# Kernel optimization log

Measured on AMD Instinct MI355X. Metric: run time of the kernel, lower is better.

## Reference

```python
import jax, jax.numpy as jnp
import numpy as np

B, C, N, T = 16, 64, 1024, 64  # batch, channels (c_in==c_out), nodes, timesteps


def setup_inputs() -> dict:
    key = jax.random.key(0)
    k = jax.random.split(key, 5)
    return {
        "x": jax.random.normal(k[0], (B, C, N, T), dtype=jnp.float32),
        "w1": jax.random.uniform(k[1], (C, C), dtype=jnp.float32),  # (c_out, c_in)
        "b1": jax.random.uniform(k[2], (C, 1), dtype=jnp.float32),  # (c_in, 1) == (c_out, 1) since c_in==c_out
        "w2": jax.random.uniform(k[3], (C, C), dtype=jnp.float32),  # (c_out, c_out)
        "b2": jax.random.uniform(k[4], (C, 1), dtype=jnp.float32),  # (c_out, 1)
    }


def reference(x, w1, b1, w2, b2):
    b, c_in, n, t = x.shape
    c_out = w1.shape[0]
    # Input transform is time-independent: batch it over all timesteps at once.
    # (c_out, c_in) x (B, c_in, N, T) -> (T, B, c_out, N), then bias-add.
    xw = jnp.einsum('vf,bfnt->tbvn', w1, x) + b1  # b1 (C,1) broadcasts over (T,B,C,N)

    def step(h, xt):
        # h: (B, c_out, N); xt: (B, c_out, N)
        new_h = jnp.tanh(xt + jnp.einsum('vu,bun->bvn', w2, h) + b2)
        return new_h, new_h

    h0 = jnp.zeros((b, c_out, n), dtype=x.dtype)
    _, out = jax.lax.scan(step, h0, xw)  # out: (T, B, c_out, N)
    return jnp.moveaxis(out, 0, 3)  # (B, c_out, N, T)
```

## Files before the change

### kernel.cpp

```cpp
#include <hip/hip_runtime.h>
#include <hip/hip_bf16.h>

namespace {
constexpr int kB = 16, kC = 64, kN = 1024, kT = 64;
constexpr size_t kWsNeed = (size_t)kB * kC * kN * kT * 4;
}

typedef short bf16x8 __attribute__((ext_vector_type(8)));
typedef float f32x4 __attribute__((ext_vector_type(4)));

__device__ __forceinline__ float tanh_fast(float x) {
    float e = __expf(2.0f * x);
    return 1.0f - 2.0f * __builtin_amdgcn_rcpf(e + 1.0f);
}

__device__ __forceinline__ unsigned short bf16_rnd(float f) {
    unsigned int u = __float_as_uint(f);
    u = (u + 0x7FFFu + ((u >> 16) & 1u)) >> 16;
    return (unsigned short)u;
}
__device__ __forceinline__ float bf16_to_f32(unsigned short s) {
    return __uint_as_float(((unsigned int)s) << 16);
}
__device__ __forceinline__ void split3(float v, unsigned short& h,
                                       unsigned short& m, unsigned short& l) {
    h = bf16_rnd(v);
    float r = v - bf16_to_f32(h);
    m = bf16_rnd(r);
    float r2 = r - bf16_to_f32(m);
    l = bf16_rnd(r2);
}


__global__ __launch_bounds__(256, 2) void xw_gemm(
    const float* __restrict__ x, const float* __restrict__ w1,
    const float* __restrict__ b1, const float* __restrict__ b2,
    float* __restrict__ ws)
{
    __shared__ __align__(16) float w1t[64][72];
    __shared__ __align__(16) float xs[16][32][20];

    const int tid = threadIdx.x;
    const int bid = blockIdx.x;
    const int tc = bid & 3;
    const int nt = (bid >> 2) & 31;
    const int b  = bid >> 7;
    const int n0 = nt * 32;

    #pragma unroll
    for (int k = 0; k < 16; ++k) {
        int idx = tid + 256 * k;
        int v = idx >> 6, f = idx & 63;
        w1t[f][v] = w1[idx];
    }

    const int vg = tid >> 5;
    const int n  = tid & 31;
    const int v0 = vg * 8;
    const int p  = (n >> 3) & 3;

    float bias[8];
    #pragma unroll
    for (int vj = 0; vj < 8; ++vj) bias[vj] = b1[v0 + vj] + b2[v0 + vj];

    float acc[8][4][4];
    #pragma unroll
    for (int vj = 0; vj < 8; ++vj)
        #pragma unroll
        for (int q = 0; q < 4; ++q)
            #pragma unroll
            for (int j = 0; j < 4; ++j) acc[vj][q][j] = bias[vj];

    for (int fc = 0; fc < 4; ++fc) {
        __syncthreads();
        #pragma unroll
        for (int r = 0; r < 8; ++r) {
            int slot = tid + 256 * r;
            int f = slot >> 7, nn = (slot >> 2) & 31, tq = slot & 3;
            const float4 xv = *reinterpret_cast<const float4*>(
                x + ((size_t)(b * 64 + fc * 16 + f) * 1024 + n0 + nn) * 64
                  + tc * 16 + tq * 4);
            int pp = (nn >> 3) & 3;
            *reinterpret_cast<float4*>(&xs[f][nn][((tq ^ pp) * 4)]) = xv;
        }
        __syncthreads();

        for (int f = 0; f < 16; ++f) {
            const int ff = fc * 16 + f;
            const float4 wA = *reinterpret_cast<const float4*>(&w1t[ff][v0]);
            const float4 wB = *reinterpret_cast<const float4*>(&w1t[ff][v0 + 4]);
            float wv[8] = {wA.x, wA.y, wA.z, wA.w, wB.x, wB.y, wB.z, wB.w};
            #pragma unroll
            for (int q = 0; q < 4; ++q) {
                const float4 xv = *reinterpret_cast<const float4*>(&xs[f][n][q * 4]);
                float xe[4] = {xv.x, xv.y, xv.z, xv.w};
                #pragma unroll
                for (int vj = 0; vj < 8; ++vj)
                    #pragma unroll
                    for (int j = 0; j < 4; ++j)
                        acc[vj][q][j] = fmaf(wv[vj], xe[j], acc[vj][q][j]);
            }
        }
    }

    const int vt  = vg >> 1;
    const int m   = n >> 4;
    const int nl  = n & 15;
    const size_t tilecol = ((size_t)(b * 32 + nt) * 64) * 2048;
    #pragma unroll
    for (int q = 0; q < 4; ++q) {
        #pragma unroll
        for (int jj = 0; jj < 4; ++jj) {
            const int t = tc * 16 + ((q ^ p) * 4) + jj;
            #pragma unroll
            for (int half = 0; half < 2; ++half) {
                const int lane = nl + 16 * ((vg & 1) * 2 + half);
                float4 o;
                o.x = acc[half * 4 + 0][q][jj];
                o.y = acc[half * 4 + 1][q][jj];
                o.z = acc[half * 4 + 2][q][jj];
                o.w = acc[half * 4 + 3][q][jj];
                size_t off = tilecol + ((size_t)t * 8 + vt * 2 + m) * 256 + lane * 4;
                *reinterpret_cast<float4*>(ws + off) = o;
            }
        }
    }
}

__global__ __launch_bounds__(256, 2) void rnn_rec(
    const float* __restrict__ w2, const float* __restrict__ ws,
    float* __restrict__ out)
{
    __shared__ __align__(16) unsigned short hsp[3][32][72];

    const int tid  = threadIdx.x;
    const int w    = tid >> 6;
    const int lane = tid & 63;
    const int lg   = lane >> 4;
    const int nl   = lane & 15;
    const int bid  = blockIdx.x;
    const int nt   = bid & 31;
    const int b    = bid >> 5;
    const int n0   = nt * 32;

    for (int i = tid; i < 3456; i += 256)
        reinterpret_cast<unsigned int*>(hsp)[i] = 0u;

    bf16x8 aw[2][3];
    #pragma unroll
    for (int kc = 0; kc < 2; ++kc) {
        const float* src = w2 + (size_t)(16 * w + nl) * 64 + kc * 32 + lg * 8;
        float wv[8];
        #pragma unroll
        for (int j = 0; j < 8; ++j) wv[j] = src[j];
        #pragma unroll
        for (int j = 0; j < 8; ++j) {
            unsigned short h, m, l;
            split3(wv[j], h, m, l);
            aw[kc][0][j] = (short)h; aw[kc][1][j] = (short)m; aw[kc][2][j] = (short)l;
        }
    }

    const size_t slab = ((size_t)(b * 32 + nt) * 64) * 2048;
    auto ldxw = [&](int t, int m) -> float4 {
        return *reinterpret_cast<const float4*>(
            ws + slab + ((size_t)t * 8 + w * 2 + m) * 256 + lane * 4);
    };

    __syncthreads();

    float4 xw0 = ldxw(0, 0), xw1 = ldxw(0, 1);
    unsigned int outw[2][4][8];

    for (int tg = 0; tg < 4; ++tg) {
        #pragma unroll
        for (int j = 0; j < 16; ++j) {
            const int t = tg * 16 + j;

            bf16x8 hb[3][2][2];
            #pragma unroll
            for (int s = 0; s < 3; ++s)
                #pragma unroll
                for (int kc = 0; kc < 2; ++kc)
                    #pragma unroll
                    for (int m = 0; m < 2; ++m)
                        hb[s][kc][m] = *reinterpret_cast<const bf16x8*>(
                            &hsp[s][nl + 16 * m][kc * 32 + lg * 8]);

            __syncthreads();

            float4 nxt0 = xw0, nxt1 = xw1;
            if (t < 63) { nxt0 = ldxw(t + 1, 0); nxt1 = ldxw(t + 1, 1); }

            f32x4 acc0 = {xw0.x, xw0.y, xw0.z, xw0.w};
            f32x4 acc1 = {xw1.x, xw1.y, xw1.z, xw1.w};
            #pragma unroll
            for (int kc = 0; kc < 2; ++kc) {
                acc0 = __builtin_amdgcn_mfma_f32_16x16x32_bf16(aw[kc][2], hb[0][kc][0], acc0, 0, 0, 0);
                acc0 = __builtin_amdgcn_mfma_f32_16x16x32_bf16(aw[kc][0], hb[2][kc][0], acc0, 0, 0, 0);
                acc0 = __builtin_amdgcn_mfma_f32_16x16x32_bf16(aw[kc][1], hb[1][kc][0], acc0, 0, 0, 0);
                acc0 = __builtin_amdgcn_mfma_f32_16x16x32_bf16(aw[kc][1], hb[0][kc][0], acc0, 0, 0, 0);
                acc0 = __builtin_amdgcn_mfma_f32_16x16x32_bf16(aw[kc][0], hb[1][kc][0], acc0, 0, 0, 0);
                acc0 = __builtin_amdgcn_mfma_f32_16x16x32_bf16(aw[kc][0], hb[0][kc][0], acc0, 0, 0, 0);
                acc1 = __builtin_amdgcn_mfma_f32_16x16x32_bf16(aw[kc][2], hb[0][kc][1], acc1, 0, 0, 0);
                acc1 = __builtin_amdgcn_mfma_f32_16x16x32_bf16(aw[kc][0], hb[2][kc][1], acc1, 0, 0, 0);
                acc1 = __builtin_amdgcn_mfma_f32_16x16x32_bf16(aw[kc][1], hb[1][kc][1], acc1, 0, 0, 0);
                acc1 = __builtin_amdgcn_mfma_f32_16x16x32_bf16(aw[kc][1], hb[0][kc][1], acc1, 0, 0, 0);
                acc1 = __builtin_amdgcn_mfma_f32_16x16x32_bf16(aw[kc][0], hb[1][kc][1], acc1, 0, 0, 0);
                acc1 = __builtin_amdgcn_mfma_f32_16x16x32_bf16(aw[kc][0], hb[0][kc][1], acc1, 0, 0, 0);
            }

            #pragma unroll
            for (int m = 0; m < 2; ++m) {
                unsigned short hs[3][4];
                #pragma unroll
                for (int r = 0; r < 4; ++r) {
                    float hv = tanh_fast(m == 0 ? acc0[r] : acc1[r]);
                    split3(hv, hs[0][r], hs[1][r], hs[2][r]);
                    if ((j & 1) == 0) outw[m][r][j >> 1] = (unsigned int)hs[0][r];
                    else              outw[m][r][j >> 1] |= ((unsigned int)hs[0][r]) << 16;
                }
                #pragma unroll
                for (int s = 0; s < 3; ++s) {
                    ushort4 pk = {hs[s][0], hs[s][1], hs[s][2], hs[s][3]};
                    *reinterpret_cast<ushort4*>(&hsp[s][nl + 16 * m][16 * w + lg * 4]) = pk;
                }
            }
            __syncthreads();

            xw0 = nxt0; xw1 = nxt1;
        }
        #pragma unroll
        for (int m = 0; m < 2; ++m) {
            #pragma unroll
            for (int r = 0; r < 4; ++r) {
                const int v = 16 * w + lg * 4 + r;
                const int nn = n0 + nl + 16 * m;
                float* dst = out + ((size_t)(b * 64 + v) * 1024 + nn) * 64 + tg * 16;
                #pragma unroll
                for (int c = 0; c < 4; ++c) {
                    float4 o;
                    o.x = bf16_to_f32((unsigned short)(outw[m][r][2 * c] & 0xFFFFu));
                    o.y = bf16_to_f32((unsigned short)(outw[m][r][2 * c] >> 16));
                    o.z = bf16_to_f32((unsigned short)(outw[m][r][2 * c + 1] & 0xFFFFu));
                    o.w = bf16_to_f32((unsigned short)(outw[m][r][2 * c + 1] >> 16));
                    *reinterpret_cast<float4*>(dst + 4 * c) = o;
                }
            }
        }
    }
}

__global__ __launch_bounds__(256, 2) void rnn_fused_kernel(
    const float* __restrict__ x, const float* __restrict__ w1,
    const float* __restrict__ b1, const float* __restrict__ w2,
    const float* __restrict__ b2, float* __restrict__ out)
{
    __shared__ __align__(16) float w1t[64][65];
    __shared__ __align__(16) float w2t[64][65];
    __shared__ __align__(16) float bsum[64];
    __shared__ __align__(16) float xs[4][64][32];
    __shared__ __align__(16) float Hs[64][32];

    const int tid = threadIdx.x;
    const int bid = blockIdx.x;
    const int b   = bid >> 5;
    const int n0  = (bid & 31) * 32;

    #pragma unroll
    for (int k = 0; k < 16; ++k) {
        const int idx = tid + 256 * k;
        const int v = idx >> 6, f = idx & 63;
        w1t[f][v] = w1[idx];
        w2t[f][v] = w2[idx];
    }
    if (tid < 64) bsum[tid] = b1[tid] + b2[tid];
    #pragma unroll
    for (int k = 0; k < 8; ++k) reinterpret_cast<float*>(Hs)[tid + 256 * k] = 0.0f;
    __syncthreads();

    const int v  = tid >> 2;
    const int ng = (tid & 3) * 8;
    const float bs = bsum[v];

    for (int tg = 0; tg < 16; ++tg) {
        #pragma unroll
        for (int k = 0; k < 8; ++k) {
            const int lin = tid + 256 * k;
            const int f = lin >> 5, n = lin & 31;
            const float4 xv = *reinterpret_cast<const float4*>(
                x + ((b * 64 + f) * 1024 + n0 + n) * 64 + tg * 4);
            xs[0][f][n] = xv.x; xs[1][f][n] = xv.y; xs[2][f][n] = xv.z; xs[3][f][n] = xv.w;
        }
        __syncthreads();
        #pragma unroll
        for (int tt = 0; tt < 4; ++tt) {
            const float* hsrc = (tt == 0) ? &Hs[0][0] : &xs[tt - 1][0][0];
            float acc[8];
            #pragma unroll
            for (int j = 0; j < 8; ++j) acc[j] = bs;
            #pragma unroll 4
            for (int f = 0; f < 64; ++f) {
                const float wv = w1t[f][v];
                const float4 xa = *reinterpret_cast<const float4*>(&xs[tt][f][ng]);
                const float4 xb = *reinterpret_cast<const float4*>(&xs[tt][f][ng + 4]);
                acc[0] = fmaf(wv, xa.x, acc[0]); acc[1] = fmaf(wv, xa.y, acc[1]);
                acc[2] = fmaf(wv, xa.z, acc[2]); acc[3] = fmaf(wv, xa.w, acc[3]);
                acc[4] = fmaf(wv, xb.x, acc[4]); acc[5] = fmaf(wv, xb.y, acc[5]);
                acc[6] = fmaf(wv, xb.z, acc[6]); acc[7] = fmaf(wv, xb.w, acc[7]);
            }
            #pragma unroll 4
            for (int u = 0; u < 64; ++u) {
                const float wv = w2t[u][v];
                const float4 ha = *reinterpret_cast<const float4*>(hsrc + u * 32 + ng);
                const float4 hb = *reinterpret_cast<const float4*>(hsrc + u * 32 + ng + 4);
                acc[0] = fmaf(wv, ha.x, acc[0]); acc[1] = fmaf(wv, ha.y, acc[1]);
                acc[2] = fmaf(wv, ha.z, acc[2]); acc[3] = fmaf(wv, ha.w, acc[3]);
                acc[4] = fmaf(wv, hb.x, acc[4]); acc[5] = fmaf(wv, hb.y, acc[5]);
                acc[6] = fmaf(wv, hb.z, acc[6]); acc[7] = fmaf(wv, hb.w, acc[7]);
            }
            float4 o0, o1;
            o0.x = tanh_fast(acc[0]); o0.y = tanh_fast(acc[1]);
            o0.z = tanh_fast(acc[2]); o0.w = tanh_fast(acc[3]);
            o1.x = tanh_fast(acc[4]); o1.y = tanh_fast(acc[5]);
            o1.z = tanh_fast(acc[6]); o1.w = tanh_fast(acc[7]);
            __syncthreads();
            *reinterpret_cast<float4*>(&xs[tt][v][ng])     = o0;
            *reinterpret_cast<float4*>(&xs[tt][v][ng + 4]) = o1;
            if (tt == 3) {
                *reinterpret_cast<float4*>(&Hs[v][ng])     = o0;
                *reinterpret_cast<float4*>(&Hs[v][ng + 4]) = o1;
            }
            __syncthreads();
        }
        #pragma unroll
        for (int k = 0; k < 8; ++k) {
            const int lin = tid + 256 * k;
            const int vv = lin >> 5, n = lin & 31;
            float4 o;
            o.x = xs[0][vv][n]; o.y = xs[1][vv][n]; o.z = xs[2][vv][n]; o.w = xs[3][vv][n];
            *reinterpret_cast<float4*>(
                out + ((b * 64 + vv) * 1024 + n0 + n) * 64 + tg * 4) = o;
        }
        __syncthreads();
    }
}

extern "C" void kernel_launch(void* const* d_in, const int* in_sizes, int n_in,
                              void* d_out, int out_size, void* d_ws, size_t ws_size,
                              hipStream_t stream) {
    const float* x  = (const float*)d_in[0];
    const float* w1 = (const float*)d_in[1];
    const float* b1 = (const float*)d_in[2];
    const float* w2 = (const float*)d_in[3];
    const float* b2 = (const float*)d_in[4];
    float* out = (float*)d_out;

    if (ws_size >= kWsNeed) {
        float* ws = (float*)d_ws;
        hipLaunchKernelGGL(xw_gemm, dim3(2048), dim3(256), 0, stream,
                           x, w1, b1, b2, ws);
        hipLaunchKernelGGL(rnn_rec, dim3(512), dim3(256), 0, stream,
                           w2, ws, out);
    } else {
        hipLaunchKernelGGL(rnn_fused_kernel, dim3(512), dim3(256), 0, stream,
                           x, w1, b1, w2, b2, out);
    }
}
```

Baseline: 640.9 us.

## Split recurrence into 16-node blocks with double-buffered swizzled LDS and packed bf16 splits

The recurrence kernel now uses 1024 blocks of 128 threads, each owning 16 nodes, so each wave computes two 16-row output tiles instead of one tile over two node groups. The hidden state buffer is double-buffered in LDS, which removes one barrier per timestep, and it is XOR-swizzled to reduce bank conflicts. The bf16 three-way split uses the packed v_cvt_pk_bf16_f32 instruction. The MFMA chains are split into two independent accumulators per tile to shorten the dependency chain. More blocks should give more parallelism on the serial recurrence, at the cost of more total weight splitting and per-block setup.

```diff
diff --git a/kernel.cpp b/kernel.cpp
--- a/kernel.cpp
+++ b/kernel.cpp
@@ -29,6 +29,25 @@
     m = bf16_rnd(r);
     float r2 = r - bf16_to_f32(m);
     l = bf16_rnd(r2);
+}
+
+__device__ __forceinline__ unsigned int cvt_pk_bf16(float a, float b) {
+    unsigned int r;
+    asm("v_cvt_pk_bf16_f32 %0, %1, %2" : "=v"(r) : "v"(a), "v"(b));
+    return r;
+}
+__device__ __forceinline__ float lof(unsigned int u) {
+    return __uint_as_float(u << 16);
+}
+__device__ __forceinline__ float hif(unsigned int u) {
+    return __uint_as_float(u & 0xffff0000u);
+}
+__device__ __forceinline__ void split3_pk(float a, float b, unsigned int& w0,
+                                          unsigned int& w1, unsigned int& w2) {
+    w0 = cvt_pk_bf16(a, b);
+    float ra = a - lof(w0), rb = b - hif(w0);
+    w1 = cvt_pk_bf16(ra, rb);
+    w2 = cvt_pk_bf16(ra - lof(w1), rb - hif(w1));
 }
 
 
@@ -127,129 +146,141 @@
     }
 }
 
-__global__ __launch_bounds__(256, 2) void rnn_rec(
+#define T6(ACC, VT, KC) \
+    ACC = __builtin_amdgcn_mfma_f32_16x16x32_bf16(aw[VT][KC][2], hb[0][KC], ACC, 0, 0, 0); \
+    ACC = __builtin_amdgcn_mfma_f32_16x16x32_bf16(aw[VT][KC][0], hb[2][KC], ACC, 0, 0, 0); \
+    ACC = __builtin_amdgcn_mfma_f32_16x16x32_bf16(aw[VT][KC][1], hb[1][KC], ACC, 0, 0, 0); \
+    ACC = __builtin_amdgcn_mfma_f32_16x16x32_bf16(aw[VT][KC][1], hb[0][KC], ACC, 0, 0, 0); \
+    ACC = __builtin_amdgcn_mfma_f32_16x16x32_bf16(aw[VT][KC][0], hb[1][KC], ACC, 0, 0, 0); \
+    ACC = __builtin_amdgcn_mfma_f32_16x16x32_bf16(aw[VT][KC][0], hb[0][KC], ACC, 0, 0, 0);
+
+#define FIN(VT, S) { \
+    float h0 = tanh_fast(S[0]), h1 = tanh_fast(S[1]); \
+    float h2 = tanh_fast(S[2]), h3 = tanh_fast(S[3]); \
+    unsigned int p0, p1, p2, q0, q1, q2; \
+    split3_pk(h0, h1, p0, p1, p2); \
+    split3_pk(h2, h3, q0, q1, q2); \
+    ow[VT][0][j] = p0; ow[VT][1][j] = q0; \
+    const int kb = (32 * w + 16 * VT + 4 * lg) ^ knl; \
+    *reinterpret_cast<uint2*>(&hsp[wbuf][0][nl][kb]) = make_uint2(p0, q0); \
+    *reinterpret_cast<uint2*>(&hsp[wbuf][1][nl][kb]) = make_uint2(p1, q1); \
+    *reinterpret_cast<uint2*>(&hsp[wbuf][2][nl][kb]) = make_uint2(p2, q2); }
+
+__global__ __launch_bounds__(128, 2) void rnn_rec(
     const float* __restrict__ w2, const float* __restrict__ ws,
     float* __restrict__ out)
 {
-    __shared__ __align__(16) unsigned short hsp[3][32][72];
+    __shared__ __align__(16) unsigned short hsp[2][3][16][72];
 
     const int tid  = threadIdx.x;
     const int w    = tid >> 6;
     const int lane = tid & 63;
     const int lg   = lane >> 4;
     const int nl   = lane & 15;
+    const int knl  = (nl & 3) << 3;
     const int bid  = blockIdx.x;
-    const int nt   = bid & 31;
-    const int b    = bid >> 5;
-    const int n0   = nt * 32;
-
-    for (int i = tid; i < 3456; i += 256)
+    const int nt16 = bid & 63;
+    const int b    = bid >> 6;
+    const int m    = nt16 & 1;
+    const int nt32 = nt16 >> 1;
+    const int n0   = nt16 * 16;
+
+    for (int i = tid; i < 3456; i += 128)
         reinterpret_cast<unsigned int*>(hsp)[i] = 0u;
 
-    bf16x8 aw[2][3];
-    #pragma unroll
-    for (int kc = 0; kc < 2; ++kc) {
-        const float* src = w2 + (size_t)(16 * w + nl) * 64 + kc * 32 + lg * 8;
-        float wv[8];
-        #pragma unroll
-        for (int j = 0; j < 8; ++j) wv[j] = src[j];
-        #pragma unroll
-        for (int j = 0; j < 8; ++j) {
-            unsigned short h, m, l;
-            split3(wv[j], h, m, l);
-            aw[kc][0][j] = (short)h; aw[kc][1][j] = (short)m; aw[kc][2][j] = (short)l;
-        }
-    }
-
-    const size_t slab = ((size_t)(b * 32 + nt) * 64) * 2048;
-    auto ldxw = [&](int t, int m) -> float4 {
-        return *reinterpret_cast<const float4*>(
-            ws + slab + ((size_t)t * 8 + w * 2 + m) * 256 + lane * 4);
-    };
+    bf16x8 aw[2][2][3];
+    #pragma unroll
+    for (int vt = 0; vt < 2; ++vt) {
+        #pragma unroll
+        for (int kc = 0; kc < 2; ++kc) {
+            const float* src = w2 + (size_t)(32 * w + 16 * vt + nl) * 64 + kc * 32 + lg * 8;
+            const float4 f0 = *reinterpret_cast<const float4*>(src);
+            const float4 f1 = *reinterpret_cast<const float4*>(src + 4);
+            float e[8] = {f0.x, f0.y, f0.z, f0.w, f1.x, f1.y, f1.z, f1.w};
+            #pragma unroll
+            for (int jp = 0; jp < 4; ++jp) {
+                unsigned int u0, u1, u2;
+                split3_pk(e[2 * jp], e[2 * jp + 1], u0, u1, u2);
+                aw[vt][kc][0][2 * jp] = (short)(u0 & 0xffffu);
+                aw[vt][kc][0][2 * jp + 1] = (short)(u0 >> 16);
+                aw[vt][kc][1][2 * jp] = (short)(u1 & 0xffffu);
+                aw[vt][kc][1][2 * jp + 1] = (short)(u1 >> 16);
+                aw[vt][kc][2][2 * jp] = (short)(u2 & 0xffffu);
+                aw[vt][kc][2][2 * jp + 1] = (short)(u2 >> 16);
+            }
+        }
+    }
+
+    const size_t slab = (size_t)(b * 32 + nt32) * 131072;
+    const float4* xq = reinterpret_cast<const float4*>(ws + slab)
+                     + (size_t)m * 64 + lane + (size_t)w * 256;
 
     __syncthreads();
 
-    float4 xw0 = ldxw(0, 0), xw1 = ldxw(0, 1);
-    unsigned int outw[2][4][8];
+    float4 xwc0 = xq[0];
+    float4 xwc1 = xq[128];
+    unsigned int ow[2][2][16];
 
     for (int tg = 0; tg < 4; ++tg) {
         #pragma unroll
         for (int j = 0; j < 16; ++j) {
             const int t = tg * 16 + j;
-
-            bf16x8 hb[3][2][2];
+            const int wbuf = t & 1, rbuf = wbuf ^ 1;
+
+            bf16x8 hb[3][2];
             #pragma unroll
             for (int s = 0; s < 3; ++s)
                 #pragma unroll
                 for (int kc = 0; kc < 2; ++kc)
-                    #pragma unroll
-                    for (int m = 0; m < 2; ++m)
-                        hb[s][kc][m] = *reinterpret_cast<const bf16x8*>(
-                            &hsp[s][nl + 16 * m][kc * 32 + lg * 8]);
+                    hb[s][kc] = *reinterpret_cast<const bf16x8*>(
+                        &hsp[rbuf][s][nl][(kc * 32 + lg * 8) ^ knl]);
+
+            float4 xn0, xn1;
+            const bool pf = (t < 63);
+            if (pf) {
+                xn0 = xq[(size_t)(t + 1) * 512];
+                xn1 = xq[(size_t)(t + 1) * 512 + 128];
+            }
+
+            f32x4 a00 = {xwc0.x, xwc0.y, xwc0.z, xwc0.w};
+            f32x4 a01 = {0.f, 0.f, 0.f, 0.f};
+            f32x4 a10 = {xwc1.x, xwc1.y, xwc1.z, xwc1.w};
+            f32x4 a11 = {0.f, 0.f, 0.f, 0.f};
+            T6(a00, 0, 0) T6(a01, 0, 1) T6(a10, 1, 0) T6(a11, 1, 1)
+            f32x4 s0 = a00 + a01;
+            f32x4 s1 = a10 + a11;
+
+            FIN(0, s0) FIN(1, s1)
 
             __syncthreads();
 
-            float4 nxt0 = xw0, nxt1 = xw1;
-            if (t < 63) { nxt0 = ldxw(t + 1, 0); nxt1 = ldxw(t + 1, 1); }
-
-            f32x4 acc0 = {xw0.x, xw0.y, xw0.z, xw0.w};
-            f32x4 acc1 = {xw1.x, xw1.y, xw1.z, xw1.w};
-            #pragma unroll
-            for (int kc = 0; kc < 2; ++kc) {
-                acc0 = __builtin_amdgcn_mfma_f32_16x16x32_bf16(aw[kc][2], hb[0][kc][0], acc0, 0, 0, 0);
-                acc0 = __builtin_amdgcn_mfma_f32_16x16x32_bf16(aw[kc][0], hb[2][kc][0], acc0, 0, 0, 0);
-                acc0 = __builtin_amdgcn_mfma_f32_16x16x32_bf16(aw[kc][1], hb[1][kc][0], acc0, 0, 0, 0);
-                acc0 = __builtin_amdgcn_mfma_f32_16x16x32_bf16(aw[kc][1], hb[0][kc][0], acc0, 0, 0, 0);
-                acc0 = __builtin_amdgcn_mfma_f32_16x16x32_bf16(aw[kc][0], hb[1][kc][0], acc0, 0, 0, 0);
-                acc0 = __builtin_amdgcn_mfma_f32_16x16x32_bf16(aw[kc][0], hb[0][kc][0], acc0, 0, 0, 0);
-                acc1 = __builtin_amdgcn_mfma_f32_16x16x32_bf16(aw[kc][2], hb[0][kc][1], acc1, 0, 0, 0);
-                acc1 = __builtin_amdgcn_mfma_f32_16x16x32_bf16(aw[kc][0], hb[2][kc][1], acc1, 0, 0, 0);
-                acc1 = __builtin_amdgcn_mfma_f32_16x16x32_bf16(aw[kc][1], hb[1][kc][1], acc1, 0, 0, 0);
-                acc1 = __builtin_amdgcn_mfma_f32_16x16x32_bf16(aw[kc][1], hb[0][kc][1], acc1, 0, 0, 0);
-                acc1 = __builtin_amdgcn_mfma_f32_16x16x32_bf16(aw[kc][0], hb[1][kc][1], acc1, 0, 0, 0);
-                acc1 = __builtin_amdgcn_mfma_f32_16x16x32_bf16(aw[kc][0], hb[0][kc][1], acc1, 0, 0, 0);
-            }
-
-            #pragma unroll
-            for (int m = 0; m < 2; ++m) {
-                unsigned short hs[3][4];
-                #pragma unroll
-                for (int r = 0; r < 4; ++r) {
-                    float hv = tanh_fast(m == 0 ? acc0[r] : acc1[r]);
-                    split3(hv, hs[0][r], hs[1][r], hs[2][r]);
-                    if ((j & 1) == 0) outw[m][r][j >> 1] = (unsigned int)hs[0][r];
-                    else              outw[m][r][j >> 1] |= ((unsigned int)hs[0][r]) << 16;
-                }
-                #pragma unroll
-                for (int s = 0; s < 3; ++s) {
-                    ushort4 pk = {hs[s][0], hs[s][1], hs[s][2], hs[s][3]};
-                    *reinterpret_cast<ushort4*>(&hsp[s][nl + 16 * m][16 * w + lg * 4]) = pk;
-                }
-            }
-            __syncthreads();
-
-            xw0 = nxt0; xw1 = nxt1;
-        }
-        #pragma unroll
-        for (int m = 0; m < 2; ++m) {
-            #pragma unroll
-            for (int r = 0; r < 4; ++r) {
-                const int v = 16 * w + lg * 4 + r;
-                const int nn = n0 + nl + 16 * m;
-                float* dst = out + ((size_t)(b * 64 + v) * 1024 + nn) * 64 + tg * 16;
+            if (pf) { xwc0 = xn0; xwc1 = xn1; }
+        }
+
+        #pragma unroll
+        for (int vt = 0; vt < 2; ++vt) {
+            #pragma unroll
+            for (int rp = 0; rp < 2; ++rp) {
+                const int v = 32 * w + 16 * vt + 4 * lg + 2 * rp;
+                float* d0 = out + ((size_t)(b * 64 + v) * 1024 + n0 + nl) * 64 + tg * 16;
+                float* d1 = d0 + 65536;
                 #pragma unroll
                 for (int c = 0; c < 4; ++c) {
-                    float4 o;
-                    o.x = bf16_to_f32((unsigned short)(outw[m][r][2 * c] & 0xFFFFu));
-                    o.y = bf16_to_f32((unsigned short)(outw[m][r][2 * c] >> 16));
-                    o.z = bf16_to_f32((unsigned short)(outw[m][r][2 * c + 1] & 0xFFFFu));
-                    o.w = bf16_to_f32((unsigned short)(outw[m][r][2 * c + 1] >> 16));
-                    *reinterpret_cast<float4*>(dst + 4 * c) = o;
+                    const unsigned int u0 = ow[vt][rp][4 * c + 0];
+                    const unsigned int u1 = ow[vt][rp][4 * c + 1];
+                    const unsigned int u2 = ow[vt][rp][4 * c + 2];
+                    const unsigned int u3 = ow[vt][rp][4 * c + 3];
+                    float4 o0 = {lof(u0), lof(u1), lof(u2), lof(u3)};
+                    float4 o1 = {hif(u0), hif(u1), hif(u2), hif(u3)};
+                    *reinterpret_cast<float4*>(d0 + 4 * c) = o0;
+                    *reinterpret_cast<float4*>(d1 + 4 * c) = o1;
                 }
             }
         }
     }
 }
+#undef T6
+#undef FIN
 
 __global__ __launch_bounds__(256, 2) void rnn_fused_kernel(
     const float* __restrict__ x, const float* __restrict__ w1,
@@ -313,11 +344,11 @@
             for (int u = 0; u < 64; ++u) {
                 const float wv = w2t[u][v];
                 const float4 ha = *reinterpret_cast<const float4*>(hsrc + u * 32 + ng);
-                const float4 hb = *reinterpret_cast<const float4*>(hsrc + u * 32 + ng + 4);
+                const float4 hb2 = *reinterpret_cast<const float4*>(hsrc + u * 32 + ng + 4);
                 acc[0] = fmaf(wv, ha.x, acc[0]); acc[1] = fmaf(wv, ha.y, acc[1]);
                 acc[2] = fmaf(wv, ha.z, acc[2]); acc[3] = fmaf(wv, ha.w, acc[3]);
-                acc[4] = fmaf(wv, hb.x, acc[4]); acc[5] = fmaf(wv, hb.y, acc[5]);
-                acc[6] = fmaf(wv, hb.z, acc[6]); acc[7] = fmaf(wv, hb.w, acc[7]);
+                acc[4] = fmaf(wv, hb2.x, acc[4]); acc[5] = fmaf(wv, hb2.y, acc[5]);
+                acc[6] = fmaf(wv, hb2.z, acc[6]); acc[7] = fmaf(wv, hb2.w, acc[7]);
             }
             float4 o0, o1;
             o0.x = tanh_fast(acc[0]); o0.y = tanh_fast(acc[1]);
@@ -360,7 +391,7 @@
         float* ws = (float*)d_ws;
         hipLaunchKernelGGL(xw_gemm, dim3(2048), dim3(256), 0, stream,
                            x, w1, b1, b2, ws);
-        hipLaunchKernelGGL(rnn_rec, dim3(512), dim3(256), 0, stream,
+        hipLaunchKernelGGL(rnn_rec, dim3(1024), dim3(128), 0, stream,
                            w2, ws, out);
     } else {
         hipLaunchKernelGGL(rnn_fused_kernel, dim3(512), dim3(256), 0, stream,
```

After: 659.1 us. +2.8%, slower.
